# Optimization experiments

Hardware: AMD Instinct MI355X
Metric: run time of the kernel (lower is better)

## Reference

```python
import jax, jax.numpy as jnp
import numpy as np

B, T, DL, DM, H = 8, 4096, 1024, 1024, 8
HD = min(DL, DM) // H  # 128


def setup_inputs() -> dict:
    key = jax.random.key(0)
    ks = jax.random.split(key, 8)
    s = 0.02

    def w(k, shape):
        return jax.random.normal(k, shape, jnp.float32) * s

    return {
        "liquid_repr": jax.random.normal(ks[0], (B, T, DL), jnp.float32),
        "mamba_repr": jax.random.normal(ks[1], (B, T, DM), jnp.float32),
        "Wlq": w(ks[2], (DL, H * HD)), "blq": jnp.zeros((H * HD,), jnp.float32),
        "Wmkv": w(ks[3], (DM, 2 * H * HD)), "bmkv": jnp.zeros((2 * H * HD,), jnp.float32),
        "Wmq": w(ks[4], (DM, H * HD)), "bmq": jnp.zeros((H * HD,), jnp.float32),
        "Wlkv": w(ks[5], (DL, 2 * H * HD)), "blkv": jnp.zeros((2 * H * HD,), jnp.float32),
        "Wlo": w(ks[6], (H * HD, DL)), "blo": jnp.zeros((DL,), jnp.float32),
        "Wmo": w(ks[7], (H * HD, DM)), "bmo": jnp.zeros((DM,), jnp.float32),
    }


def _attn(q, k, v):
    # q,k,v: [B,T,H,HD]. Faithful to torch: matmul over last two dims ->
    # scores [B,T,H,H] (attention over the heads axis per timestep).
    scores = jnp.einsum('bthd,btgd->bthg', q, k) / jnp.sqrt(jnp.float32(HD))
    w = jax.nn.softmax(scores, axis=-1)
    return jnp.einsum('bthg,btgd->bthd', w, v)


def reference(liquid_repr, mamba_repr, Wlq, blq, Wmkv, bmkv, Wmq, bmq,
              Wlkv, blkv, Wlo, blo, Wmo, bmo):
    b, t, _ = liquid_repr.shape
    # liquid queries mamba
    q_l = (liquid_repr @ Wlq + blq).reshape(b, t, H, HD)
    kv_m = (mamba_repr @ Wmkv + bmkv).reshape(b, t, H, 2 * HD)
    k_m, v_m = kv_m[..., :HD], kv_m[..., HD:]
    a_l = _attn(q_l, k_m, v_m).reshape(b, t, H * HD)
    enhanced_liquid = liquid_repr + a_l @ Wlo + blo
    # mamba queries liquid
    q_m = (mamba_repr @ Wmq + bmq).reshape(b, t, H, HD)
    kv_l = (liquid_repr @ Wlkv + blkv).reshape(b, t, H, 2 * HD)
    k_l, v_l = kv_l[..., :HD], kv_l[..., HD:]
    a_m = _attn(q_m, k_l, v_l).reshape(b, t, H * HD)
    enhanced_mamba = mamba_repr + a_m @ Wmo + bmo
    return enhanced_liquid, enhanced_mamba
```

## Files before the change

kernel.cpp:

```cpp
#include <hip/hip_runtime.h>

typedef unsigned short u16;
typedef unsigned int u32;

typedef __attribute__((ext_vector_type(4))) float floatx4;
typedef __attribute__((ext_vector_type(8))) __bf16 bf16x8;

typedef __attribute__((address_space(3))) u32 lds_u32_t;
typedef __attribute__((address_space(1))) u32 glb_u32_t;

__device__ __forceinline__ void gld_lds16(const u16* g, u16* l) {
    __builtin_amdgcn_global_load_lds((glb_u32_t*)g, (lds_u32_t*)l, 16, 0, 0);
}

__device__ __forceinline__ u16 f2bf(float f) {
    u32 u = __float_as_uint(f);
    u += 0x7fffu + ((u >> 16) & 1u);
    return (u16)(u >> 16);
}
__device__ __forceinline__ u32 pk2(float a, float b) {
    u32 x = __float_as_uint(a), y = __float_as_uint(b);
    x += 0x7fffu + ((x >> 16) & 1u);
    y += 0x7fffu + ((y >> 16) & 1u);
    return (x >> 16) | (y & 0xffff0000u);
}
__device__ __forceinline__ float bl(u32 u) { return __uint_as_float(u << 16); }
__device__ __forceinline__ float bh(u32 u) { return __uint_as_float(u & 0xffff0000u); }

#define SWZ(d) ((d) ^ ((((d) >> 7) & 7) << 4))

#define BM 128
#define BN 128
#define BK 64

__global__ __launch_bounds__(256) void convert_f32_bf16(
    const float* __restrict__ src, u16* __restrict__ dst)
{
    const size_t i = ((size_t)blockIdx.x * 256 + threadIdx.x) * 8;
    float4 a = *(const float4*)(src + i);
    float4 b = *(const float4*)(src + i + 4);
    *(uint4*)(dst + i) = make_uint4(pk2(a.x, a.y), pk2(a.z, a.w),
                                    pk2(b.x, b.y), pk2(b.z, b.w));
}

__device__ __forceinline__ void remap_bmbn(int nbn, int& bm, int& bn) {
    const int nwg = (int)gridDim.x;
    const int flat = (int)blockIdx.x;
    const int wg = (flat & 7) * (nwg >> 3) + (flat >> 3);
    bn = wg % nbn;
    bm = wg / nbn;
}

__global__ __launch_bounds__(256, 2) void gemm_a16_c16(
    const u16* __restrict__ A, int lda,
    const u16* __restrict__ Bt,
    const float* __restrict__ bias,
    u16* __restrict__ C, int ldc,
    int K, int nbn)
{
    __shared__ __align__(16) u16 sA[BM * BK];
    __shared__ __align__(16) u16 sB[BN * BK];
    const int tid  = threadIdx.x;
    int bm, bn; remap_bmbn(nbn, bm, bn);
    const int lane = tid & 63,  wave = tid >> 6;
    const int wm   = wave >> 1, wn   = wave & 1;
    const int l15  = lane & 15, quad = lane >> 4;
    const char* sAb = (const char*)sA;
    const char* sBb = (const char*)sB;

    floatx4 acc[4][4] = {};

    for (int k0 = 0; k0 < K; k0 += BK) {
        __syncthreads();
#pragma unroll
        for (int j = 0; j < 4; ++j) {
            const int clin = tid + j * 256;
            const int csrc = clin ^ ((clin >> 3) & 7);
            const int r = csrc >> 3, c = (csrc & 7) * 8;
            gld_lds16(A  + (size_t)(bm * BM + r) * lda + k0 + c, &sA[clin * 8]);
            gld_lds16(Bt + (size_t)(bn * BN + r) * K   + k0 + c, &sB[clin * 8]);
        }
        __syncthreads();

#pragma unroll
        for (int ks = 0; ks < 2; ++ks) {
            bf16x8 af[4], bfr[4];
#pragma unroll
            for (int mi = 0; mi < 4; mi++)
                af[mi] = *(const bf16x8*)(sAb +
                    SWZ((wm * 64 + mi * 16 + l15) * 128 + ks * 64 + quad * 16));
#pragma unroll
            for (int ni = 0; ni < 4; ni++)
                bfr[ni] = *(const bf16x8*)(sBb +
                    SWZ((wn * 64 + ni * 16 + l15) * 128 + ks * 64 + quad * 16));
#pragma unroll
            for (int mi = 0; mi < 4; mi++)
#pragma unroll
                for (int ni = 0; ni < 4; ni++)
                    acc[mi][ni] = __builtin_amdgcn_mfma_f32_16x16x32_bf16(
                        af[mi], bfr[ni], acc[mi][ni], 0, 0, 0);
        }
    }

    const int row0 = bm * BM + wm * 64 + quad * 4;
    const int col0 = bn * BN + wn * 64 + l15;
#pragma unroll
    for (int mi = 0; mi < 4; mi++) {
#pragma unroll
        for (int ni = 0; ni < 4; ni++) {
            const int col = col0 + ni * 16;
            const float bv = bias[col];
#pragma unroll
            for (int r = 0; r < 4; r++) {
                const int row = row0 + mi * 16 + r;
                C[(size_t)row * ldc + col] = f2bf(acc[mi][ni][r] + bv);
            }
        }
    }
}

__global__ __launch_bounds__(256, 2) void gemm_a16_c32(
    const u16* __restrict__ A, int lda,
    const u16* __restrict__ Bt,
    const float* __restrict__ bias,
    const float* __restrict__ R, int ldr,
    float* __restrict__ C, int ldc,
    int K, int nbn)
{
    __shared__ __align__(16) u16 sA[BM * BK];
    __shared__ __align__(16) u16 sB[BN * BK];
    const int tid  = threadIdx.x;
    int bm, bn; remap_bmbn(nbn, bm, bn);
    const int lane = tid & 63,  wave = tid >> 6;
    const int wm   = wave >> 1, wn   = wave & 1;
    const int l15  = lane & 15, quad = lane >> 4;
    const char* sAb = (const char*)sA;
    const char* sBb = (const char*)sB;

    floatx4 acc[4][4] = {};

    for (int k0 = 0; k0 < K; k0 += BK) {
        __syncthreads();
#pragma unroll
        for (int j = 0; j < 4; ++j) {
            const int clin = tid + j * 256;
            const int csrc = clin ^ ((clin >> 3) & 7);
            const int r = csrc >> 3, c = (csrc & 7) * 8;
            gld_lds16(A  + (size_t)(bm * BM + r) * lda + k0 + c, &sA[clin * 8]);
            gld_lds16(Bt + (size_t)(bn * BN + r) * K   + k0 + c, &sB[clin * 8]);
        }
        __syncthreads();

#pragma unroll
        for (int ks = 0; ks < 2; ++ks) {
            bf16x8 af[4], bfr[4];
#pragma unroll
            for (int mi = 0; mi < 4; mi++)
                af[mi] = *(const bf16x8*)(sAb +
                    SWZ((wm * 64 + mi * 16 + l15) * 128 + ks * 64 + quad * 16));
#pragma unroll
            for (int ni = 0; ni < 4; ni++)
                bfr[ni] = *(const bf16x8*)(sBb +
                    SWZ((wn * 64 + ni * 16 + l15) * 128 + ks * 64 + quad * 16));
#pragma unroll
            for (int mi = 0; mi < 4; mi++)
#pragma unroll
                for (int ni = 0; ni < 4; ni++)
                    acc[mi][ni] = __builtin_amdgcn_mfma_f32_16x16x32_bf16(
                        af[mi], bfr[ni], acc[mi][ni], 0, 0, 0);
        }
    }

    const int row0 = bm * BM + wm * 64 + quad * 4;
    const int col0 = bn * BN + wn * 64 + l15;
#pragma unroll
    for (int mi = 0; mi < 4; mi++) {
#pragma unroll
        for (int ni = 0; ni < 4; ni++) {
            const int col = col0 + ni * 16;
            const float bv = bias[col];
#pragma unroll
            for (int r = 0; r < 4; r++) {
                const int row = row0 + mi * 16 + r;
                C[(size_t)row * ldc + col] =
                    acc[mi][ni][r] + bv + R[(size_t)row * ldr + col];
            }
        }
    }
}

__global__ __launch_bounds__(256) void attn8(
    const u16* Q,
    const u16* __restrict__ KV,
    u16* O,
    int qstride, int kvstride)
{
    const int wid = threadIdx.x >> 6, lane = threadIdx.x & 63;
    const size_t pos = (size_t)blockIdx.x * 4 + wid;
    const u16* qrow  = Q  + pos * qstride;
    const u16* kvrow = KV + pos * kvstride;
    const int h = lane >> 3, g = lane & 7;

    const u16* qh = qrow  + h * 128;
    const u16* kg = kvrow + g * 256;
    float s0 = 0.f, s1 = 0.f, s2 = 0.f, s3 = 0.f;
#pragma unroll
    for (int j = 0; j < 16; ++j) {
        uint4 qa = *(const uint4*)(qh + j * 8);
        uint4 ka = *(const uint4*)(kg + j * 8);
        s0 += bl(qa.x) * bl(ka.x);  s1 += bh(qa.x) * bh(ka.x);
        s2 += bl(qa.y) * bl(ka.y);  s3 += bh(qa.y) * bh(ka.y);
        s0 += bl(qa.z) * bl(ka.z);  s1 += bh(qa.z) * bh(ka.z);
        s2 += bl(qa.w) * bl(ka.w);  s3 += bh(qa.w) * bh(ka.w);
    }
    float s = ((s0 + s1) + (s2 + s3)) * 0.08838834764831845f;

    float m = s;
    m = fmaxf(m, __shfl_xor(m, 1, 64));
    m = fmaxf(m, __shfl_xor(m, 2, 64));
    m = fmaxf(m, __shfl_xor(m, 4, 64));
    float p = __expf(s - m);
    float sum = p;
    sum += __shfl_xor(sum, 1, 64);
    sum += __shfl_xor(sum, 2, 64);
    sum += __shfl_xor(sum, 4, 64);
    const float w = p / sum;

    const int db = g;
    float o[16];
#pragma unroll
    for (int j = 0; j < 16; ++j) o[j] = 0.f;
    const u16* vbase = kvrow + 128 + db * 16;
#pragma unroll
    for (int gg = 0; gg < 8; ++gg) {
        const float wv = __shfl(w, h * 8 + gg, 64);
        const u16* vp = vbase + gg * 256;
        uint4 va = *(const uint4*)(vp);
        uint4 vb = *(const uint4*)(vp + 8);
        o[0]  += wv * bl(va.x);  o[1]  += wv * bh(va.x);
        o[2]  += wv * bl(va.y);  o[3]  += wv * bh(va.y);
        o[4]  += wv * bl(va.z);  o[5]  += wv * bh(va.z);
        o[6]  += wv * bl(va.w);  o[7]  += wv * bh(va.w);
        o[8]  += wv * bl(vb.x);  o[9]  += wv * bh(vb.x);
        o[10] += wv * bl(vb.y);  o[11] += wv * bh(vb.y);
        o[12] += wv * bl(vb.z);  o[13] += wv * bh(vb.z);
        o[14] += wv * bl(vb.w);  o[15] += wv * bh(vb.w);
    }

    u16* orow = O + pos * qstride + h * 128 + db * 16;
    u32 pk[8];
#pragma unroll
    for (int j = 0; j < 8; ++j)
        pk[j] = pk2(o[2 * j], o[2 * j + 1]);
    ((uint4*)orow)[0] = make_uint4(pk[0], pk[1], pk[2], pk[3]);
    ((uint4*)orow)[1] = make_uint4(pk[4], pk[5], pk[6], pk[7]);
}

__global__ __launch_bounds__(256) void transpose_f32_bf16(
    const float* __restrict__ src, u16* __restrict__ dst, int K, int N)
{
    __shared__ float tile[32][33];
    const int tx = threadIdx.x & 31, ty = threadIdx.x >> 5;
    const int c0 = blockIdx.x * 32, r0 = blockIdx.y * 32;
#pragma unroll
    for (int i = 0; i < 4; i++)
        tile[ty + i * 8][tx] = src[(size_t)(r0 + ty + i * 8) * N + c0 + tx];
    __syncthreads();
#pragma unroll
    for (int i = 0; i < 4; i++)
        dst[(size_t)(c0 + ty + i * 8) * K + r0 + tx] = f2bf(tile[tx][ty + i * 8]);
}

extern "C" void kernel_launch(void* const* d_in, const int* in_sizes, int n_in,
                              void* d_out, int out_size, void* d_ws, size_t ws_size,
                              hipStream_t stream) {
    const float* liquid = (const float*)d_in[0];
    const float* mamba  = (const float*)d_in[1];
    const float* Wlq  = (const float*)d_in[2];
    const float* blq  = (const float*)d_in[3];
    const float* Wmkv = (const float*)d_in[4];
    const float* bmkv = (const float*)d_in[5];
    const float* Wmq  = (const float*)d_in[6];
    const float* bmq  = (const float*)d_in[7];
    const float* Wlkv = (const float*)d_in[8];
    const float* blkv = (const float*)d_in[9];
    const float* Wlo  = (const float*)d_in[10];
    const float* blo  = (const float*)d_in[11];
    const float* Wmo  = (const float*)d_in[12];
    const float* bmo  = (const float*)d_in[13];
    float* out = (float*)d_out;

    u16* p = (u16*)d_ws;
    u16* WtLq  = p; p += (size_t)1024 * 1024;
    u16* WtLkv = p; p += (size_t)2048 * 1024;
    u16* WtMq  = p; p += (size_t)1024 * 1024;
    u16* WtMkv = p; p += (size_t)2048 * 1024;
    u16* WtLo  = p; p += (size_t)1024 * 1024;
    u16* WtMo  = p; p += (size_t)1024 * 1024;
    u16* Q  = p; p += (size_t)32768 * 1024;
    u16* KV = p;

    u16* Lb = (u16*)(out + (size_t)32768 * 1024);
    u16* Mb = Lb + (size_t)32768 * 1024;

    transpose_f32_bf16<<<dim3(32, 32), 256, 0, stream>>>(Wlq,  WtLq,  1024, 1024);
    transpose_f32_bf16<<<dim3(64, 32), 256, 0, stream>>>(Wlkv, WtLkv, 1024, 2048);
    transpose_f32_bf16<<<dim3(32, 32), 256, 0, stream>>>(Wmq,  WtMq,  1024, 1024);
    transpose_f32_bf16<<<dim3(64, 32), 256, 0, stream>>>(Wmkv, WtMkv, 1024, 2048);
    transpose_f32_bf16<<<dim3(32, 32), 256, 0, stream>>>(Wlo,  WtLo,  1024, 1024);
    transpose_f32_bf16<<<dim3(32, 32), 256, 0, stream>>>(Wmo,  WtMo,  1024, 1024);

    convert_f32_bf16<<<16384, 256, 0, stream>>>(liquid, Lb);
    convert_f32_bf16<<<16384, 256, 0, stream>>>(mamba,  Mb);

    gemm_a16_c16<<<2048, 256, 0, stream>>>(Lb, 1024, WtLq,  blq,  Q,  1024, 1024, 8);
    gemm_a16_c16<<<4096, 256, 0, stream>>>(Mb, 1024, WtMkv, bmkv, KV, 2048, 1024, 16);
    attn8<<<8192, 256, 0, stream>>>(Q, KV, Q, 1024, 2048);
    gemm_a16_c32<<<2048, 256, 0, stream>>>(Q, 1024, WtLo, blo, liquid, 1024,
                                           out, 1024, 1024, 8);

    gemm_a16_c16<<<2048, 256, 0, stream>>>(Mb, 1024, WtMq,  bmq,  Q,  1024, 1024, 8);
    gemm_a16_c16<<<4096, 256, 0, stream>>>(Lb, 1024, WtLkv, blkv, KV, 2048, 1024, 16);
    attn8<<<8192, 256, 0, stream>>>(Q, KV, Q, 1024, 2048);
    gemm_a16_c32<<<2048, 256, 0, stream>>>(Q, 1024, WtMo, bmo, mamba, 1024,
                                           out + (size_t)32768 * 1024, 1024, 1024, 8);
}
```

Before: 1.370 ms.

## Enlarge GEMM M-tile to 256 rows and merge transpose/convert launches

Doubles the GEMM block tile along M from 128 to 256, so each wave computes a 128x64 sub-tile with 32 accumulators and reuses each B fragment across twice as many MFMAs. Grid sizes are halved to match. The six weight transposes are merged into one launch via blockIdx.z, and the two activation conversions into one launch, to cut launch overhead. The larger tile raises register pressure (128 accumulator VGPRs per lane) under launch_bounds(256,2) and doubles A LDS usage, which may cost occupancy or cause spills.

```diff
diff --git a/kernel.cpp b/kernel.cpp
--- a/kernel.cpp
+++ b/kernel.cpp
@@ -29,18 +29,22 @@
 
 #define SWZ(d) ((d) ^ ((((d) >> 7) & 7) << 4))
 
-#define BM 128
+#define BM 256
 #define BN 128
 #define BK 64
 
-__global__ __launch_bounds__(256) void convert_f32_bf16(
-    const float* __restrict__ src, u16* __restrict__ dst)
-{
-    const size_t i = ((size_t)blockIdx.x * 256 + threadIdx.x) * 8;
-    float4 a = *(const float4*)(src + i);
-    float4 b = *(const float4*)(src + i + 4);
-    *(uint4*)(dst + i) = make_uint4(pk2(a.x, a.y), pk2(a.z, a.w),
-                                    pk2(b.x, b.y), pk2(b.z, b.w));
+__global__ __launch_bounds__(256) void convert2_f32_bf16(
+    const float* __restrict__ s0, u16* __restrict__ d0,
+    const float* __restrict__ s1, u16* __restrict__ d1)
+{
+    const size_t half = (size_t)16384 * 256 * 8;
+    size_t i = ((size_t)blockIdx.x * 256 + threadIdx.x) * 8;
+    const float* s = s0; u16* d = d0;
+    if (i >= half) { i -= half; s = s1; d = d1; }
+    float4 a = *(const float4*)(s + i);
+    float4 b = *(const float4*)(s + i + 4);
+    *(uint4*)(d + i) = make_uint4(pk2(a.x, a.y), pk2(a.z, a.w),
+                                  pk2(b.x, b.y), pk2(b.z, b.w));
 }
 
 __device__ __forceinline__ void remap_bmbn(int nbn, int& bm, int& bn) {
@@ -49,6 +53,26 @@
     const int wg = (flat & 7) * (nwg >> 3) + (flat >> 3);
     bn = wg % nbn;
     bm = wg / nbn;
+}
+
+__device__ __forceinline__ void stage_tiles(
+    const u16* __restrict__ A, int lda, const u16* __restrict__ Bt, int K,
+    int bm, int bn, int k0, u16* sA, u16* sB, int tid)
+{
+#pragma unroll
+    for (int j = 0; j < 8; ++j) {
+        const int clin = tid + j * 256;
+        const int csrc = clin ^ ((clin >> 3) & 7);
+        const int r = csrc >> 3, c = (csrc & 7) * 8;
+        gld_lds16(A + (size_t)(bm * BM + r) * lda + k0 + c, &sA[clin * 8]);
+    }
+#pragma unroll
+    for (int j = 0; j < 4; ++j) {
+        const int clin = tid + j * 256;
+        const int csrc = clin ^ ((clin >> 3) & 7);
+        const int r = csrc >> 3, c = (csrc & 7) * 8;
+        gld_lds16(Bt + (size_t)(bn * BN + r) * K + k0 + c, &sB[clin * 8]);
+    }
 }
 
 __global__ __launch_bounds__(256, 2) void gemm_a16_c16(
@@ -68,33 +92,26 @@
     const char* sAb = (const char*)sA;
     const char* sBb = (const char*)sB;
 
-    floatx4 acc[4][4] = {};
+    floatx4 acc[8][4] = {};
 
     for (int k0 = 0; k0 < K; k0 += BK) {
         __syncthreads();
-#pragma unroll
-        for (int j = 0; j < 4; ++j) {
-            const int clin = tid + j * 256;
-            const int csrc = clin ^ ((clin >> 3) & 7);
-            const int r = csrc >> 3, c = (csrc & 7) * 8;
-            gld_lds16(A  + (size_t)(bm * BM + r) * lda + k0 + c, &sA[clin * 8]);
-            gld_lds16(Bt + (size_t)(bn * BN + r) * K   + k0 + c, &sB[clin * 8]);
-        }
+        stage_tiles(A, lda, Bt, K, bm, bn, k0, sA, sB, tid);
         __syncthreads();
 
 #pragma unroll
         for (int ks = 0; ks < 2; ++ks) {
-            bf16x8 af[4], bfr[4];
-#pragma unroll
-            for (int mi = 0; mi < 4; mi++)
+            bf16x8 af[8], bfr[4];
+#pragma unroll
+            for (int mi = 0; mi < 8; mi++)
                 af[mi] = *(const bf16x8*)(sAb +
-                    SWZ((wm * 64 + mi * 16 + l15) * 128 + ks * 64 + quad * 16));
+                    SWZ((wm * 128 + mi * 16 + l15) * 128 + ks * 64 + quad * 16));
 #pragma unroll
             for (int ni = 0; ni < 4; ni++)
                 bfr[ni] = *(const bf16x8*)(sBb +
                     SWZ((wn * 64 + ni * 16 + l15) * 128 + ks * 64 + quad * 16));
 #pragma unroll
-            for (int mi = 0; mi < 4; mi++)
+            for (int mi = 0; mi < 8; mi++)
 #pragma unroll
                 for (int ni = 0; ni < 4; ni++)
                     acc[mi][ni] = __builtin_amdgcn_mfma_f32_16x16x32_bf16(
@@ -102,10 +119,10 @@
         }
     }
 
-    const int row0 = bm * BM + wm * 64 + quad * 4;
+    const int row0 = bm * BM + wm * 128 + quad * 4;
     const int col0 = bn * BN + wn * 64 + l15;
 #pragma unroll
-    for (int mi = 0; mi < 4; mi++) {
+    for (int mi = 0; mi < 8; mi++) {
 #pragma unroll
         for (int ni = 0; ni < 4; ni++) {
             const int col = col0 + ni * 16;
@@ -137,33 +154,26 @@
     const char* sAb = (const char*)sA;
     const char* sBb = (const char*)sB;
 
-    floatx4 acc[4][4] = {};
+    floatx4 acc[8][4] = {};
 
     for (int k0 = 0; k0 < K; k0 += BK) {
         __syncthreads();
-#pragma unroll
-        for (int j = 0; j < 4; ++j) {
-            const int clin = tid + j * 256;
-            const int csrc = clin ^ ((clin >> 3) & 7);
-            const int r = csrc >> 3, c = (csrc & 7) * 8;
-            gld_lds16(A  + (size_t)(bm * BM + r) * lda + k0 + c, &sA[clin * 8]);
-            gld_lds16(Bt + (size_t)(bn * BN + r) * K   + k0 + c, &sB[clin * 8]);
-        }
+        stage_tiles(A, lda, Bt, K, bm, bn, k0, sA, sB, tid);
         __syncthreads();
 
 #pragma unroll
         for (int ks = 0; ks < 2; ++ks) {
-            bf16x8 af[4], bfr[4];
-#pragma unroll
-            for (int mi = 0; mi < 4; mi++)
+            bf16x8 af[8], bfr[4];
+#pragma unroll
+            for (int mi = 0; mi < 8; mi++)
                 af[mi] = *(const bf16x8*)(sAb +
-                    SWZ((wm * 64 + mi * 16 + l15) * 128 + ks * 64 + quad * 16));
+                    SWZ((wm * 128 + mi * 16 + l15) * 128 + ks * 64 + quad * 16));
 #pragma unroll
             for (int ni = 0; ni < 4; ni++)
                 bfr[ni] = *(const bf16x8*)(sBb +
                     SWZ((wn * 64 + ni * 16 + l15) * 128 + ks * 64 + quad * 16));
 #pragma unroll
-            for (int mi = 0; mi < 4; mi++)
+            for (int mi = 0; mi < 8; mi++)
 #pragma unroll
                 for (int ni = 0; ni < 4; ni++)
                     acc[mi][ni] = __builtin_amdgcn_mfma_f32_16x16x32_bf16(
@@ -171,10 +181,10 @@
         }
     }
 
-    const int row0 = bm * BM + wm * 64 + quad * 4;
+    const int row0 = bm * BM + wm * 128 + quad * 4;
     const int col0 = bn * BN + wn * 64 + l15;
 #pragma unroll
-    for (int mi = 0; mi < 4; mi++) {
+    for (int mi = 0; mi < 8; mi++) {
 #pragma unroll
         for (int ni = 0; ni < 4; ni++) {
             const int col = col0 + ni * 16;
@@ -256,12 +266,27 @@
     ((uint4*)orow)[1] = make_uint4(pk[4], pk[5], pk[6], pk[7]);
 }
 
-__global__ __launch_bounds__(256) void transpose_f32_bf16(
-    const float* __restrict__ src, u16* __restrict__ dst, int K, int N)
-{
+__global__ __launch_bounds__(256) void transpose6_f32_bf16(
+    const float* __restrict__ s0, u16* __restrict__ d0, int n0,
+    const float* __restrict__ s1, u16* __restrict__ d1, int n1,
+    const float* __restrict__ s2, u16* __restrict__ d2, int n2,
+    const float* __restrict__ s3, u16* __restrict__ d3, int n3,
+    const float* __restrict__ s4, u16* __restrict__ d4, int n4,
+    const float* __restrict__ s5, u16* __restrict__ d5, int n5)
+{
+    const float* srcs[6] = {s0, s1, s2, s3, s4, s5};
+    u16*         dsts[6] = {d0, d1, d2, d3, d4, d5};
+    const int    ns[6]   = {n0, n1, n2, n3, n4, n5};
+    const int z = blockIdx.z;
+    const int N = ns[z];
+    const int c0 = blockIdx.x * 32;
+    if (c0 >= N) return;
+    const float* src = srcs[z];
+    u16* dst = dsts[z];
+    const int K = 1024;
     __shared__ float tile[32][33];
     const int tx = threadIdx.x & 31, ty = threadIdx.x >> 5;
-    const int c0 = blockIdx.x * 32, r0 = blockIdx.y * 32;
+    const int r0 = blockIdx.y * 32;
 #pragma unroll
     for (int i = 0; i < 4; i++)
         tile[ty + i * 8][tx] = src[(size_t)(r0 + ty + i * 8) * N + c0 + tx];
@@ -303,25 +328,25 @@
     u16* Lb = (u16*)(out + (size_t)32768 * 1024);
     u16* Mb = Lb + (size_t)32768 * 1024;
 
-    transpose_f32_bf16<<<dim3(32, 32), 256, 0, stream>>>(Wlq,  WtLq,  1024, 1024);
-    transpose_f32_bf16<<<dim3(64, 32), 256, 0, stream>>>(Wlkv, WtLkv, 1024, 2048);
-    transpose_f32_bf16<<<dim3(32, 32), 256, 0, stream>>>(Wmq,  WtMq,  1024, 1024);
-    transpose_f32_bf16<<<dim3(64, 32), 256, 0, stream>>>(Wmkv, WtMkv, 1024, 2048);
-    transpose_f32_bf16<<<dim3(32, 32), 256, 0, stream>>>(Wlo,  WtLo,  1024, 1024);
-    transpose_f32_bf16<<<dim3(32, 32), 256, 0, stream>>>(Wmo,  WtMo,  1024, 1024);
-
-    convert_f32_bf16<<<16384, 256, 0, stream>>>(liquid, Lb);
-    convert_f32_bf16<<<16384, 256, 0, stream>>>(mamba,  Mb);
-
-    gemm_a16_c16<<<2048, 256, 0, stream>>>(Lb, 1024, WtLq,  blq,  Q,  1024, 1024, 8);
-    gemm_a16_c16<<<4096, 256, 0, stream>>>(Mb, 1024, WtMkv, bmkv, KV, 2048, 1024, 16);
+    transpose6_f32_bf16<<<dim3(64, 32, 6), 256, 0, stream>>>(
+        Wlq,  WtLq,  1024,
+        Wlkv, WtLkv, 2048,
+        Wmq,  WtMq,  1024,
+        Wmkv, WtMkv, 2048,
+        Wlo,  WtLo,  1024,
+        Wmo,  WtMo,  1024);
+
+    convert2_f32_bf16<<<32768, 256, 0, stream>>>(liquid, Lb, mamba, Mb);
+
+    gemm_a16_c16<<<1024, 256, 0, stream>>>(Lb, 1024, WtLq,  blq,  Q,  1024, 1024, 8);
+    gemm_a16_c16<<<2048, 256, 0, stream>>>(Mb, 1024, WtMkv, bmkv, KV, 2048, 1024, 16);
     attn8<<<8192, 256, 0, stream>>>(Q, KV, Q, 1024, 2048);
-    gemm_a16_c32<<<2048, 256, 0, stream>>>(Q, 1024, WtLo, blo, liquid, 1024,
+    gemm_a16_c32<<<1024, 256, 0, stream>>>(Q, 1024, WtLo, blo, liquid, 1024,
                                            out, 1024, 1024, 8);
 
-    gemm_a16_c16<<<2048, 256, 0, stream>>>(Mb, 1024, WtMq,  bmq,  Q,  1024, 1024, 8);
-    gemm_a16_c16<<<4096, 256, 0, stream>>>(Lb, 1024, WtLkv, blkv, KV, 2048, 1024, 16);
+    gemm_a16_c16<<<1024, 256, 0, stream>>>(Mb, 1024, WtMq,  bmq,  Q,  1024, 1024, 8);
+    gemm_a16_c16<<<2048, 256, 0, stream>>>(Lb, 1024, WtLkv, blkv, KV, 2048, 1024, 16);
     attn8<<<8192, 256, 0, stream>>>(Q, KV, Q, 1024, 2048);
-    gemm_a16_c32<<<2048, 256, 0, stream>>>(Q, 1024, WtMo, bmo, mamba, 1024,
+    gemm_a16_c32<<<1024, 256, 0, stream>>>(Q, 1024, WtMo, bmo, mamba, 1024,
                                            out + (size_t)32768 * 1024, 1024, 1024, 8);
 }
```

Measured after the change: 1.309 ms. 4.4% less time.
